# Optimization experiments

Hardware: AMD Instinct MI355X
Metric: run time of the kernel (lower is better)

Reference implementation:

```python
import jax, jax.numpy as jnp
import numpy as np

EPS = 1e-3  # keras LayerNormalization default epsilon

def _layernorm(x, g, b):
    mu = jnp.mean(x, axis=-1, keepdims=True)
    var = jnp.mean(jnp.square(x - mu), axis=-1, keepdims=True)
    return (x - mu) * jax.lax.rsqrt(var + EPS) * g + b

def setup_inputs() -> dict:
    key = jax.random.key(0)
    ks = jax.random.split(key, 12)
    B, T, C = 2, 2048, 768
    s = 0.02
    return {
        "x": jax.random.normal(ks[0], (B, T, C), jnp.float32),
        "ln1_g": jnp.ones((C,), jnp.float32), "ln1_b": jnp.zeros((C,), jnp.float32),
        "Wq": jax.random.normal(ks[1], (C, C), jnp.float32) * s, "bq": jnp.zeros((C,), jnp.float32),
        "Wk": jax.random.normal(ks[2], (C, C), jnp.float32) * s, "bk": jnp.zeros((C,), jnp.float32),
        "Wv": jax.random.normal(ks[3], (C, C), jnp.float32) * s, "bv": jnp.zeros((C,), jnp.float32),
        "ln2_g": jnp.ones((C,), jnp.float32), "ln2_b": jnp.zeros((C,), jnp.float32),
        "W1": jax.random.normal(ks[4], (C, 4 * C), jnp.float32) * s, "b1": jnp.zeros((4 * C,), jnp.float32),
        "W2": jax.random.normal(ks[5], (4 * C, C), jnp.float32) * s, "b2": jnp.zeros((C,), jnp.float32),
    }

def reference(x, ln1_g, ln1_b, Wq, bq, Wk, bk, Wv, bv, ln2_g, ln2_b, W1, b1, W2, b2):
    H = 12
    B, T, C = x.shape
    dh = C // H
    # pre-LN (note: original overwrites x with LN output before residual)
    x = _layernorm(x, ln1_g, ln1_b)
    q = (x @ Wq + bq).reshape(B, T, H, dh).transpose(0, 2, 1, 3)
    k = (x @ Wk + bk).reshape(B, T, H, dh).transpose(0, 2, 1, 3)
    v = (x @ Wv + bv).reshape(B, T, H, dh).transpose(0, 2, 1, 3)
    # original computes K @ Q^T (transpose_b on query)
    scores = jnp.einsum('bhid,bhjd->bhij', k, q) / jnp.sqrt(jnp.float32(dh))
    mask = jnp.tril(jnp.ones((T, T), bool))
    scores = jnp.where(mask, scores, -jnp.inf)
    p = jax.nn.softmax(scores, axis=-1)
    y = jnp.einsum('bhij,bhjd->bhid', p, v)  # [B,H,T,dh]
    y = y.transpose(0, 2, 1, 3).reshape(B, T, C)
    x = x + y
    h = _layernorm(x, ln2_g, ln2_b)
    h = jax.nn.gelu(h @ W1 + b1, approximate=False)
    h = h @ W2 + b2
    return x + h
```

## Files before the change

### kernel.cpp

```cpp
#include <hip/hip_runtime.h>
#include <hip/hip_bf16.h>
#include <cmath>


#define BB 2
#define TT 2048
#define CC 768
#define HH 12
#define DH 64
#define NROWS (BB*TT)
#define NHEADS (BB*HH)

typedef __attribute__((ext_vector_type(8))) short bf16x8;
typedef __attribute__((ext_vector_type(4))) float f32x4;
typedef __attribute__((ext_vector_type(4))) unsigned short u16x4;

__device__ __forceinline__ unsigned short f2bf(float f){
  union { __hip_bfloat16 h; unsigned short u; } c;
  c.h = __float2bfloat16(f);
  return c.u;
}
__device__ __forceinline__ float bf2f(unsigned short u){
  union { unsigned int i; float f; } x; x.i = ((unsigned int)u) << 16; return x.f;
}
template<int BK>
__device__ __forceinline__ int swzk(int r, int c){
  if constexpr (BK == 64) return (r << 6) + (c ^ ((r & 7) << 3));
  else                    return (r << 5) + (c ^ (((r >> 1) & 3) << 3));
}
template<int BK>
__device__ __forceinline__ int swzsrc(int r, int c){
  if constexpr (BK == 64) return c ^ ((r & 7) << 3);
  else                    return c ^ (((r >> 1) & 3) << 3);
}
__device__ __forceinline__ float wred_sum(float v){
  #pragma unroll
  for(int m = 1; m < 64; m <<= 1) v += __shfl_xor(v, m, 64);
  return v;
}
__device__ __forceinline__ float gelu_fast(float x){
  float x2 = x * x;
  float e = x * fmaf(x2, 0.044715f, 1.0f) * 2.30203136f;
  float t = exp2f(e);
  return x - x / (t + 1.0f);
}
__device__ __forceinline__ void gload_lds16(const void* g, void* l){
  __builtin_amdgcn_global_load_lds((const __attribute__((address_space(1))) void*)g,
                                   (__attribute__((address_space(3))) void*)l, 16, 0, 0);
}
template<int N> __device__ __forceinline__ void waitcnt_vm(){
  if constexpr (N == 0)      asm volatile("s_waitcnt vmcnt(0)" ::: "memory");
  else if constexpr (N == 4) asm volatile("s_waitcnt vmcnt(4)" ::: "memory");
  else if constexpr (N == 8) asm volatile("s_waitcnt vmcnt(8)" ::: "memory");
  else static_assert(N == 0 || N == 4 || N == 8, "unsupported vmcnt");
}

#define SCLOG2 (0.125f * 1.44269504f)

__device__ __forceinline__ void tc_body(const float* __restrict__ in,
                                        unsigned short* __restrict__ out,
                                        int K, int N, int bx, int by,
                                        float (*tile)[33]){
  int n0 = bx * 32, k0 = by * 32;
  int t = threadIdx.x; int c = t & 31; int r0 = t >> 5;
  #pragma unroll
  for(int p = 0; p < 4; p++){
    int r = r0 + p * 8;
    tile[r][c] = in[(size_t)(k0 + r) * N + n0 + c];
  }
  __syncthreads();
  #pragma unroll
  for(int p = 0; p < 4; p++){
    int r = r0 + p * 8;
    out[(size_t)(n0 + r) * K + k0 + c] = f2bf(tile[c][r]);
  }
}

__device__ __forceinline__ void ln_body(const float* __restrict__ in,
                                        const float* __restrict__ gm,
                                        const float* __restrict__ bt,
                                        unsigned short* __restrict__ out_b,
                                        int r){
  int t = threadIdx.x;
  const float* row = in + (size_t)r * CC;
  float v0 = row[t], v1 = row[t + 256], v2 = row[t + 512];
  float s = wred_sum(v0 + v1 + v2);
  __shared__ float red[4];
  if((t & 63) == 0) red[t >> 6] = s;
  __syncthreads();
  float mu = (red[0] + red[1] + red[2] + red[3]) * (1.0f / CC);
  float d0 = v0 - mu, d1 = v1 - mu, d2 = v2 - mu;
  float q = wred_sum(d0 * d0 + d1 * d1 + d2 * d2);
  __shared__ float red2[4];
  if((t & 63) == 0) red2[t >> 6] = q;
  __syncthreads();
  float var = (red2[0] + red2[1] + red2[2] + red2[3]) * (1.0f / CC);
  float rinv = rsqrtf(var + 1e-3f);
  float o0 = d0 * rinv * gm[t]       + bt[t];
  float o1 = d1 * rinv * gm[t + 256] + bt[t + 256];
  float o2 = d2 * rinv * gm[t + 512] + bt[t + 512];
  size_t base = (size_t)r * CC;
  out_b[base + t] = f2bf(o0); out_b[base + t + 256] = f2bf(o1); out_b[base + t + 512] = f2bf(o2);
}

__global__ __launch_bounds__(256) void prep_ln_kernel(const float* __restrict__ Wq,
                                                      const float* __restrict__ Wk,
                                                      const float* __restrict__ Wv,
                                                      const float* __restrict__ W1,
                                                      const float* __restrict__ W2,
                                                      const float* __restrict__ bq,
                                                      const float* __restrict__ bk,
                                                      const float* __restrict__ bv,
                                                      const float* __restrict__ x,
                                                      const float* __restrict__ ln1g,
                                                      const float* __restrict__ ln1b,
                                                      unsigned short* __restrict__ wqkv,
                                                      unsigned short* __restrict__ w1t,
                                                      unsigned short* __restrict__ w2t,
                                                      float* __restrict__ bqkv,
                                                      unsigned short* __restrict__ xlnb){
  __shared__ float tile[32][33];
  int o = blockIdx.x;
  if(o < 1728){
    int z = o / 576, r = o % 576;
    const float* in = (z == 0) ? Wq : (z == 1) ? Wk : Wv;
    tc_body(in, wqkv + (size_t)z * CC * CC, CC, CC, r % 24, r / 24, tile);
  } else if(o < 4032){
    int r = o - 1728;
    tc_body(W1, w1t, CC, 4 * CC, r % 96, r / 96, tile);
  } else if(o < 6336){
    int r = o - 4032;
    tc_body(W2, w2t, 4 * CC, CC, r % 24, r / 24, tile);
  } else if(o < 6345){
    int i = (o - 6336) * 256 + threadIdx.x;
    if(i < 3 * CC) bqkv[i] = (i < CC) ? bq[i] : (i < 2 * CC) ? bk[i - CC] : bv[i - 2 * CC];
  } else {
    ln_body(x, ln1g, ln1b, xlnb, o - 6345);
  }
}

template<int MODE, int TILE, int BK>
__global__ __launch_bounds__(256) void gemm_bt(const unsigned short* __restrict__ A,
                                               const unsigned short* __restrict__ Bt,
                                               const float* __restrict__ bias,
                                               const float* __restrict__ resid,
                                               void* __restrict__ outp,
                                               unsigned short* __restrict__ vt,
                                               int M, int N, int K){
  constexpr int F = TILE / 32;
  constexpr int SEGS = TILE * BK / 512;
  constexpr int R = SEGS / 4;
  constexpr int NLD = 2 * R;
  constexpr int LPR = BK / 8;
  constexpr int RPS = 512 / BK;
  __shared__ unsigned short As[3][TILE * BK];
  __shared__ unsigned short Bs[3][TILE * BK];
  int m0 = blockIdx.y * TILE, n0 = blockIdx.x * TILE;
  int t = threadIdx.x; int w = t >> 6; int l = t & 63;
  int g = l >> 4; int lc = l & 15;
  int wm = w >> 1, wn = w & 1;
  f32x4 zero4 = {0.f, 0.f, 0.f, 0.f};
  f32x4 acc[F][F];
  #pragma unroll
  for(int mi = 0; mi < F; mi++)
    #pragma unroll
    for(int ni = 0; ni < F; ni++) acc[mi][ni] = zero4;

  auto stage = [&](int ks, int cb){
    #pragma unroll
    for(int p = 0; p < R; p++){
      int sgi = w * R + p;
      int r = sgi * RPS + l / LPR;
      int c = (l % LPR) * 8;
      int csrc = swzsrc<BK>(r, c);
      gload_lds16(A  + (size_t)(m0 + r) * K + ks + csrc, &As[cb][sgi * 512]);
      gload_lds16(Bt + (size_t)(n0 + r) * K + ks + csrc, &Bs[cb][sgi * 512]);
    }
  };

  int nt = K / BK;
  stage(0, 0);
  if(nt > 1) stage(BK, 1);
  if(nt > 2) stage(2 * BK, 2);
  int cur = 0;
  for(int ti = 0; ti < nt; ti++){
    if(ti + 2 < nt)      waitcnt_vm<2 * NLD>();
    else if(ti + 1 < nt) waitcnt_vm<NLD>();
    else                 waitcnt_vm<0>();
    __builtin_amdgcn_s_barrier();
    #pragma unroll
    for(int kk = 0; kk < BK / 32; kk++){
      bf16x8 af[F], bfv[F];
      #pragma unroll
      for(int mi = 0; mi < F; mi++) af[mi]  = *(const bf16x8*)&As[cur][swzk<BK>(wm * (TILE / 2) + mi * 16 + lc, kk * 32 + g * 8)];
      #pragma unroll
      for(int ni = 0; ni < F; ni++) bfv[ni] = *(const bf16x8*)&Bs[cur][swzk<BK>(wn * (TILE / 2) + ni * 16 + lc, kk * 32 + g * 8)];
      #pragma unroll
      for(int mi = 0; mi < F; mi++)
        #pragma unroll
        for(int ni = 0; ni < F; ni++)
          acc[mi][ni] = __builtin_amdgcn_mfma_f32_16x16x32_bf16(af[mi], bfv[ni], acc[mi][ni], 0, 0, 0);
    }
    __builtin_amdgcn_s_barrier();
    if(ti + 3 < nt) stage((ti + 3) * BK, cur);
    cur = (cur == 2) ? 0 : cur + 1;
  }
  #pragma unroll
  for(int mi = 0; mi < F; mi++)
    #pragma unroll
    for(int ni = 0; ni < F; ni++){
      int col = n0 + wn * (TILE / 2) + ni * 16 + lc;
      float bvv = bias[col];
      if(MODE == 3 && col >= 2 * CC){
        int hh = (col - 2 * CC) >> 6, d = (col - 2 * CC) & 63;
        int rowb = m0 + wm * (TILE / 2) + mi * 16 + g * 4;
        int bb = rowb >> 11, tb = rowb & 2047;
        u16x4 pk;
        #pragma unroll
        for(int rr = 0; rr < 4; rr++) pk[rr] = f2bf(acc[mi][ni][rr] + bvv);
        *(u16x4*)&vt[(((size_t)bb * HH + hh) * DH + d) * TT + tb] = pk;
      } else {
        #pragma unroll
        for(int rr = 0; rr < 4; rr++){
          int row = m0 + wm * (TILE / 2) + mi * 16 + g * 4 + rr;
          float v = acc[mi][ni][rr] + bvv;
          size_t idx = (size_t)row * N + col;
          if(MODE == 2) ((float*)outp)[idx] = v + resid[idx];
          else          ((unsigned short*)outp)[idx] = f2bf(v);
        }
      }
    }
}

__global__ __launch_bounds__(512, 2) void gemm256_gelu(const unsigned short* __restrict__ A,
                                                       const unsigned short* __restrict__ Bt,
                                                       const float* __restrict__ bias,
                                                       unsigned short* __restrict__ outp,
                                                       int M, int N, int K){
  __shared__ unsigned short As[2][256 * 32];
  __shared__ unsigned short Bs[2][256 * 32];
  int m0 = blockIdx.y * 256, n0 = blockIdx.x * 256;
  int t = threadIdx.x; int w = t >> 6; int l = t & 63;
  int g = l >> 4; int lc = l & 15;
  int wm = w >> 2, wn = w & 3;
  f32x4 zero4 = {0.f, 0.f, 0.f, 0.f};
  f32x4 acc[8][4];
  #pragma unroll
  for(int mi = 0; mi < 8; mi++)
    #pragma unroll
    for(int ni = 0; ni < 4; ni++) acc[mi][ni] = zero4;

  auto stage = [&](int ks, int cb){
    #pragma unroll
    for(int p = 0; p < 2; p++){
      int sgi = w * 2 + p;
      int r = sgi * 16 + (l >> 2);
      int c = (l & 3) * 8;
      int csrc = swzsrc<32>(r, c);
      gload_lds16(A  + (size_t)(m0 + r) * K + ks + csrc, &As[cb][sgi * 512]);
      gload_lds16(Bt + (size_t)(n0 + r) * K + ks + csrc, &Bs[cb][sgi * 512]);
    }
  };

  int nt = K >> 5;
  stage(0, 0);
  if(nt > 1) stage(32, 1);
  for(int ti = 0; ti < nt; ti++){
    if(ti + 1 < nt) waitcnt_vm<4>(); else waitcnt_vm<0>();
    __builtin_amdgcn_s_barrier();
    int cur = ti & 1;
    bf16x8 af[8], bfv[4];
    #pragma unroll
    for(int mi = 0; mi < 8; mi++) af[mi]  = *(const bf16x8*)&As[cur][swzk<32>(wm * 128 + mi * 16 + lc, g * 8)];
    #pragma unroll
    for(int ni = 0; ni < 4; ni++) bfv[ni] = *(const bf16x8*)&Bs[cur][swzk<32>(wn * 64 + ni * 16 + lc, g * 8)];
    #pragma unroll
    for(int mi = 0; mi < 8; mi++)
      #pragma unroll
      for(int ni = 0; ni < 4; ni++)
        acc[mi][ni] = __builtin_amdgcn_mfma_f32_16x16x32_bf16(af[mi], bfv[ni], acc[mi][ni], 0, 0, 0);
    __builtin_amdgcn_s_barrier();
    if(ti + 2 < nt) stage((ti + 2) * 32, cur);
  }
  #pragma unroll
  for(int mi = 0; mi < 8; mi++)
    #pragma unroll
    for(int ni = 0; ni < 4; ni++){
      int col = n0 + wn * 64 + ni * 16 + lc;
      float bvv = bias[col];
      #pragma unroll
      for(int rr = 0; rr < 4; rr++){
        int row = m0 + wm * 128 + mi * 16 + g * 4 + rr;
        outp[(size_t)row * N + col] = f2bf(gelu_fast(acc[mi][ni][rr] + bvv));
      }
    }
}

__global__ __launch_bounds__(256) void attn_kernel(const unsigned short* __restrict__ qkv,
                                                   const unsigned short* __restrict__ vt,
                                                   unsigned short* __restrict__ po,
                                                   float* __restrict__ pl,
                                                   float* __restrict__ pm){
  __shared__ unsigned short Aq[2][64 * 64];
  __shared__ unsigned short Vs[2][64 * 64];
  __shared__ unsigned short Ps[4][16 * 64];
  int o = blockIdx.x;
  int xcd = o & 7, qq = o >> 3;
  int head = xcd * 3 + (qq % 3);
  int r_ = qq / 3;
  int bx = 31 - (r_ >> 1);
  int sp = r_ & 1;
  int b = head / HH, h = head % HH;
  int t = threadIdx.x; int w = t >> 6; int l = t & 63;
  int g = l >> 4, lc = l & 15;
  int i0w = bx * 64 + w * 16;
  int irow = i0w + lc;
  unsigned short* pw = &Ps[w][0];

  int hh = (bx + 2) >> 1;
  int js0 = sp ? hh : 0;
  int js1 = sp ? (bx + 1) : hh;

  int rl = l >> 3;
  int csrc = ((l & 7) * 8) ^ (rl * 8);

  bf16x8 bk[2];
  #pragma unroll
  for(int kk = 0; kk < 2; kk++)
    bk[kk] = *(const bf16x8*)(qkv + (size_t)(b * TT + irow) * (3 * CC) + CC + h * DH + kk * 32 + g * 8);

  float m_ = 0.0f, lsum = 0.f;
  f32x4 zero4 = {0.f, 0.f, 0.f, 0.f};
  f32x4 o4[4];
  #pragma unroll
  for(int ds = 0; ds < 4; ds++) o4[ds] = zero4;

  auto stage = [&](int j0, int cb){
    #pragma unroll
    for(int p = 0; p < 2; p++){
      int sgi = w * 2 + p;
      int row = sgi * 8 + rl;
      gload_lds16(qkv + (size_t)(b * TT + j0 + row) * (3 * CC) + h * DH + csrc, &Aq[cb][sgi * 512]);
      gload_lds16(vt  + (size_t)(head * DH + row) * TT + j0 + csrc,             &Vs[cb][sgi * 512]);
    }
  };

  if(js0 < js1){
    stage(js0 * 64, js0 & 1);
    if(js0 + 1 < js1) stage((js0 + 1) * 64, (js0 + 1) & 1);

    for(int jt = js0; jt < js1; jt++){
      int j0 = jt * 64;
      int buf = jt & 1;
      if(jt + 1 < js1) waitcnt_vm<4>(); else waitcnt_vm<0>();
      __builtin_amdgcn_s_barrier();
      f32x4 s[4];
      __builtin_amdgcn_s_setprio(1);
      #pragma unroll
      for(int js = 0; js < 4; js++){
        s[js] = zero4;
        #pragma unroll
        for(int kk = 0; kk < 2; kk++){
          bf16x8 aq = *(const bf16x8*)&Aq[buf][swzk<64>(js * 16 + lc, kk * 32 + g * 8)];
          s[js] = __builtin_amdgcn_mfma_f32_16x16x32_bf16(aq, bk[kk], s[js], 0, 0, 0);
        }
      }
      __builtin_amdgcn_s_setprio(0);
      if(j0 + 63 > i0w){
        #pragma unroll
        for(int js = 0; js < 4; js++)
          #pragma unroll
          for(int rr = 0; rr < 4; rr++){
            int j = j0 + js * 16 + g * 4 + rr;
            if(j > irow) s[js][rr] = -1e30f;
          }
      }
      float nmSC = -m_ * SCLOG2;
      f32x4 p[4];
      float rsum = 0.f;
      #pragma unroll
      for(int js = 0; js < 4; js++)
        #pragma unroll
        for(int rr = 0; rr < 4; rr++){
          float pv = exp2f(fmaf(s[js][rr], SCLOG2, nmSC));
          p[js][rr] = pv;
          rsum += pv;
        }
      rsum += __shfl_xor(rsum, 16, 64);
      rsum += __shfl_xor(rsum, 32, 64);
      if(__builtin_expect(__any(!(rsum < 1e30f)), 0)){
        float mx = -1e30f;
        #pragma unroll
        for(int js = 0; js < 4; js++)
          #pragma unroll
          for(int rr = 0; rr < 4; rr++) mx = fmaxf(mx, s[js][rr]);
        mx = fmaxf(mx, __shfl_xor(mx, 16, 64));
        mx = fmaxf(mx, __shfl_xor(mx, 32, 64));
        float mn = fmaxf(m_, mx);
        float al = exp2f((m_ - mn) * SCLOG2);
        m_ = mn;
        lsum *= al;
        #pragma unroll
        for(int rr = 0; rr < 4; rr++){
          float alb = __shfl(al, g * 4 + rr, 64);
          #pragma unroll
          for(int ds = 0; ds < 4; ds++) o4[ds][rr] *= alb;
        }
        nmSC = -m_ * SCLOG2;
        rsum = 0.f;
        #pragma unroll
        for(int js = 0; js < 4; js++)
          #pragma unroll
          for(int rr = 0; rr < 4; rr++){
            float pv = exp2f(fmaf(s[js][rr], SCLOG2, nmSC));
            p[js][rr] = pv;
            rsum += pv;
          }
        rsum += __shfl_xor(rsum, 16, 64);
        rsum += __shfl_xor(rsum, 32, 64);
      }
      lsum += rsum;
      #pragma unroll
      for(int js = 0; js < 4; js++){
        u16x4 pk;
        #pragma unroll
        for(int rr = 0; rr < 4; rr++) pk[rr] = f2bf(p[js][rr]);
        *(u16x4*)&pw[swzk<64>(lc, js * 16 + g * 4)] = pk;
      }
      bf16x8 pa[2];
      #pragma unroll
      for(int kk = 0; kk < 2; kk++)
        pa[kk] = *(const bf16x8*)&pw[swzk<64>(lc, kk * 32 + g * 8)];
      __builtin_amdgcn_s_setprio(1);
      #pragma unroll
      for(int ds = 0; ds < 4; ds++)
        #pragma unroll
        for(int kk = 0; kk < 2; kk++){
          bf16x8 vb = *(const bf16x8*)&Vs[buf][swzk<64>(ds * 16 + lc, kk * 32 + g * 8)];
          o4[ds] = __builtin_amdgcn_mfma_f32_16x16x32_bf16(pa[kk], vb, o4[ds], 0, 0, 0);
        }
      __builtin_amdgcn_s_setprio(0);
      __builtin_amdgcn_s_barrier();
      if(jt + 2 < js1) stage((jt + 2) * 64, buf);
    }
  }
  size_t pobase = (size_t)sp * (NHEADS * TT * DH) + (size_t)head * TT * DH;
  #pragma unroll
  for(int rr = 0; rr < 4; rr++){
    int ig = i0w + g * 4 + rr;
    #pragma unroll
    for(int ds = 0; ds < 4; ds++)
      po[pobase + (size_t)ig * DH + ds * 16 + lc] = f2bf(o4[ds][rr]);
  }
  if(g == 0){
    size_t pidx = (size_t)sp * (NHEADS * TT) + (size_t)head * TT + i0w + lc;
    pl[pidx] = lsum;
    pm[pidx] = m_;
  }
}

__global__ __launch_bounds__(256) void combine_ln2(const unsigned short* __restrict__ po,
                                                   const float* __restrict__ pl,
                                                   const float* __restrict__ pm,
                                                   const unsigned short* __restrict__ xlnb,
                                                   const float* __restrict__ gm,
                                                   const float* __restrict__ bt,
                                                   float* __restrict__ x1,
                                                   unsigned short* __restrict__ hln2){
  int r = blockIdx.x; int t = threadIdx.x;
  int b = r >> 11, i = r & 2047;
  float v[3];
  #pragma unroll
  for(int p = 0; p < 3; p++){
    int c = t + p * 256;
    int h = c >> 6, d = c & 63;
    size_t pidx = ((size_t)(b * HH + h)) * TT + i;
    float m0v = pm[pidx], m1v = pm[pidx + NHEADS * TT];
    float l0 = pl[pidx],  l1 = pl[pidx + NHEADS * TT];
    float M = fmaxf(m0v, m1v);
    float w0 = exp2f((m0v - M) * SCLOG2), w1 = exp2f((m1v - M) * SCLOG2);
    float p0 = bf2f(po[pidx * DH + d]);
    float p1 = bf2f(po[(size_t)NHEADS * TT * DH + pidx * DH + d]);
    float att = (p0 * w0 + p1 * w1) / (l0 * w0 + l1 * w1);
    v[p] = bf2f(xlnb[(size_t)r * CC + c]) + att;
  }
  float s = wred_sum(v[0] + v[1] + v[2]);
  __shared__ float red[4];
  if((t & 63) == 0) red[t >> 6] = s;
  __syncthreads();
  float mu = (red[0] + red[1] + red[2] + red[3]) * (1.0f / CC);
  float d0 = v[0] - mu, d1 = v[1] - mu, d2 = v[2] - mu;
  float q = wred_sum(d0 * d0 + d1 * d1 + d2 * d2);
  __shared__ float red2[4];
  if((t & 63) == 0) red2[t >> 6] = q;
  __syncthreads();
  float var = (red2[0] + red2[1] + red2[2] + red2[3]) * (1.0f / CC);
  float rinv = rsqrtf(var + 1e-3f);
  size_t base = (size_t)r * CC;
  x1[base + t] = v[0]; x1[base + t + 256] = v[1]; x1[base + t + 512] = v[2];
  hln2[base + t]       = f2bf(d0 * rinv * gm[t]       + bt[t]);
  hln2[base + t + 256] = f2bf(d1 * rinv * gm[t + 256] + bt[t + 256]);
  hln2[base + t + 512] = f2bf(d2 * rinv * gm[t + 512] + bt[t + 512]);
}

extern "C" void kernel_launch(void* const* d_in, const int* in_sizes, int n_in,
                              void* d_out, int out_size, void* d_ws, size_t ws_size,
                              hipStream_t stream){
  const float* x    = (const float*)d_in[0];
  const float* ln1g = (const float*)d_in[1];
  const float* ln1b = (const float*)d_in[2];
  const float* Wq   = (const float*)d_in[3];
  const float* bq   = (const float*)d_in[4];
  const float* Wk   = (const float*)d_in[5];
  const float* bk   = (const float*)d_in[6];
  const float* Wv   = (const float*)d_in[7];
  const float* bv   = (const float*)d_in[8];
  const float* ln2g = (const float*)d_in[9];
  const float* ln2b = (const float*)d_in[10];
  const float* W1   = (const float*)d_in[11];
  const float* b1   = (const float*)d_in[12];
  const float* W2   = (const float*)d_in[13];
  const float* b2   = (const float*)d_in[14];

  char* ws = (char*)d_ws;
  unsigned short* po   = (unsigned short*)(ws + 0);
  unsigned short* xlnb = (unsigned short*)(ws + 12582912);
  float*          x1   = (float*)(ws + 18874368);
  unsigned short* hln2 = (unsigned short*)(ws + 31457280);
  unsigned short* wqkv = (unsigned short*)(ws + 37748736);
  float*          bqkv = (float*)(ws + 41287680);
  unsigned short* w1t  = (unsigned short*)(ws + 41296896);
  unsigned short* w2t  = (unsigned short*)(ws + 46015488);
  unsigned short* qkv  = (unsigned short*)(ws + 50734080);
  unsigned short* vt   = (unsigned short*)(ws + 69608448);
  float*          pl   = (float*)(ws + 75899904);
  float*          pm   = (float*)(ws + 76293120);
  unsigned short* mlp1 = (unsigned short*)(ws + 50734080);

  prep_ln_kernel<<<dim3(6345 + NROWS), 256, 0, stream>>>(Wq, Wk, Wv, W1, W2, bq, bk, bv,
                                                         x, ln1g, ln1b,
                                                         wqkv, w1t, w2t, bqkv, xlnb);

  gemm_bt<3, 128, 32><<<dim3(18, 32), 256, 0, stream>>>(xlnb, wqkv, bqkv, nullptr, qkv, vt, NROWS, 3 * CC, CC);

  attn_kernel<<<dim3(1536), 256, 0, stream>>>(qkv, vt, po, pl, pm);

  combine_ln2<<<dim3(NROWS), 256, 0, stream>>>(po, pl, pm, xlnb, ln2g, ln2b, x1, hln2);

  gemm256_gelu<<<dim3(12, 16), 512, 0, stream>>>(hln2, w1t, b1, mlp1, NROWS, 4 * CC, CC);

  gemm_bt<2, 64, 64><<<dim3(12, 64), 256, 0, stream>>>(mlp1, w2t, b2, x1, d_out, nullptr, NROWS, CC, 4 * CC);

  (void)in_sizes; (void)n_in; (void)out_size; (void)ws_size;
}
```

Measured before the change: 163.2 us.

## Restructure MLP1 GEMM into eight-phase pipelined loop with finer-grained LDS staging

Replaces the two-stage K-loop of the 256x256 GELU GEMM with an 8-phase schedule. Each 64-wide K tile is split into two 32-wide halves, and LDS reads, global-to-LDS loads and MFMA quads are interleaved across phases with barriers and s_setprio around the MFMA blocks. It keeps up to four half-tiles in flight (vmcnt(6)) so global loads, LDS reads and matrix math overlap more tightly. In exchange it adds more barriers per K step and more LDS (2x2x8192 per operand), and it depends on precise waitcnt accounting.

```diff
diff --git a/kernel.cpp b/kernel.cpp
--- a/kernel.cpp
+++ b/kernel.cpp
@@ -51,8 +51,9 @@
 template<int N> __device__ __forceinline__ void waitcnt_vm(){
   if constexpr (N == 0)      asm volatile("s_waitcnt vmcnt(0)" ::: "memory");
   else if constexpr (N == 4) asm volatile("s_waitcnt vmcnt(4)" ::: "memory");
+  else if constexpr (N == 6) asm volatile("s_waitcnt vmcnt(6)" ::: "memory");
   else if constexpr (N == 8) asm volatile("s_waitcnt vmcnt(8)" ::: "memory");
-  else static_assert(N == 0 || N == 4 || N == 8, "unsupported vmcnt");
+  else static_assert(N == 0 || N == 4 || N == 6 || N == 8, "unsupported vmcnt");
 }
 
 #define SCLOG2 (0.125f * 1.44269504f)
@@ -232,13 +233,33 @@
     }
 }
 
-__global__ __launch_bounds__(512, 2) void gemm256_gelu(const unsigned short* __restrict__ A,
-                                                       const unsigned short* __restrict__ Bt,
-                                                       const float* __restrict__ bias,
-                                                       unsigned short* __restrict__ outp,
-                                                       int M, int N, int K){
-  __shared__ unsigned short As[2][256 * 32];
-  __shared__ unsigned short Bs[2][256 * 32];
+#define SWZ32(r, c) (((r) << 5) + ((c) ^ ((((r) >> 1) & 3) << 3)))
+#define MFMA_QUAD(MIB)                                                          \
+  _Pragma("unroll") for(int q = 0; q < 4; q++){                                 \
+    _Pragma("unroll") for(int ni = 0; ni < 4; ni++)                             \
+      acc[(MIB) + q][ni] = __builtin_amdgcn_mfma_f32_16x16x32_bf16(             \
+          af[q], bfv[ni], acc[(MIB) + q][ni], 0, 0, 0); }
+#define LOAD_A(BUF, KH, MIB)                                                    \
+  _Pragma("unroll") for(int q = 0; q < 4; q++)                                  \
+    af[q] = *(const bf16x8*)&As[BUF][KH][SWZ32(wm * 128 + ((MIB) + q) * 16 + lc, g * 8)];
+#define LOAD_B(BUF, KH)                                                         \
+  _Pragma("unroll") for(int q = 0; q < 4; q++)                                  \
+    bfv[q] = *(const bf16x8*)&Bs[BUF][KH][SWZ32(wn * 64 + q * 16 + lc, g * 8)];
+#define PH_TAIL                                                                 \
+  __builtin_amdgcn_s_barrier();                                                 \
+  asm volatile("s_waitcnt lgkmcnt(0)" ::: "memory");                            \
+  __builtin_amdgcn_s_setprio(1);
+#define PH_END                                                                  \
+  __builtin_amdgcn_s_setprio(0);                                                \
+  __builtin_amdgcn_s_barrier();
+
+__global__ __launch_bounds__(512, 2) void gemm256_8ph(const unsigned short* __restrict__ A,
+                                                      const unsigned short* __restrict__ Bt,
+                                                      const float* __restrict__ bias,
+                                                      unsigned short* __restrict__ outp,
+                                                      int M, int N, int K){
+  __shared__ unsigned short As[2][2][8192];
+  __shared__ unsigned short Bs[2][2][8192];
   int m0 = blockIdx.y * 256, n0 = blockIdx.x * 256;
   int t = threadIdx.x; int w = t >> 6; int l = t & 63;
   int g = l >> 4; int lc = l & 15;
@@ -250,37 +271,62 @@
     #pragma unroll
     for(int ni = 0; ni < 4; ni++) acc[mi][ni] = zero4;
 
-  auto stage = [&](int ks, int cb){
+  auto stageH = [&](const unsigned short* __restrict__ X, int rowbase, int kt, int kh,
+                    unsigned short* slot){
     #pragma unroll
     for(int p = 0; p < 2; p++){
-      int sgi = w * 2 + p;
-      int r = sgi * 16 + (l >> 2);
-      int c = (l & 3) * 8;
-      int csrc = swzsrc<32>(r, c);
-      gload_lds16(A  + (size_t)(m0 + r) * K + ks + csrc, &As[cb][sgi * 512]);
-      gload_lds16(Bt + (size_t)(n0 + r) * K + ks + csrc, &Bs[cb][sgi * 512]);
+      int r = p * 128 + (t >> 2);
+      int c = (t & 3) * 8;
+      int csrc = c ^ (((r >> 1) & 3) << 3);
+      gload_lds16(X + (size_t)(rowbase + r) * K + kt * 64 + kh * 32 + csrc,
+                  slot + p * 4096 + w * 512);
     }
   };
 
-  int nt = K >> 5;
-  stage(0, 0);
-  if(nt > 1) stage(32, 1);
-  for(int ti = 0; ti < nt; ti++){
-    if(ti + 1 < nt) waitcnt_vm<4>(); else waitcnt_vm<0>();
-    __builtin_amdgcn_s_barrier();
-    int cur = ti & 1;
-    bf16x8 af[8], bfv[4];
-    #pragma unroll
-    for(int mi = 0; mi < 8; mi++) af[mi]  = *(const bf16x8*)&As[cur][swzk<32>(wm * 128 + mi * 16 + lc, g * 8)];
-    #pragma unroll
-    for(int ni = 0; ni < 4; ni++) bfv[ni] = *(const bf16x8*)&Bs[cur][swzk<32>(wn * 64 + ni * 16 + lc, g * 8)];
-    #pragma unroll
-    for(int mi = 0; mi < 8; mi++)
-      #pragma unroll
-      for(int ni = 0; ni < 4; ni++)
-        acc[mi][ni] = __builtin_amdgcn_mfma_f32_16x16x32_bf16(af[mi], bfv[ni], acc[mi][ni], 0, 0, 0);
-    __builtin_amdgcn_s_barrier();
-    if(ti + 2 < nt) stage((ti + 2) * 32, cur);
+  int nt = K >> 6;
+  int niter = nt >> 1;
+  bf16x8 af[4], bfv[4];
+
+  stageH(A,  m0, 0, 0, &As[0][0][0]);
+  stageH(Bt, n0, 0, 0, &Bs[0][0][0]);
+  stageH(A,  m0, 0, 1, &As[0][1][0]);
+  stageH(Bt, n0, 0, 1, &Bs[0][1][0]);
+  stageH(Bt, n0, 1, 0, &Bs[1][0][0]);
+  stageH(A,  m0, 1, 0, &As[1][0][0]);
+  stageH(Bt, n0, 1, 1, &Bs[1][1][0]);
+  waitcnt_vm<6>();
+  __builtin_amdgcn_s_barrier();
+
+  for(int i = 0; i < niter; i++){
+    int t2 = 2 * i + 2, t3 = 2 * i + 3;
+    bool s2 = t2 < nt, s3 = t3 < nt;
+    bool last = (i == niter - 1);
+    LOAD_A(0, 0, 0) LOAD_B(0, 0)
+    stageH(A, m0, 2 * i + 1, 1, &As[1][1][0]);
+    PH_TAIL MFMA_QUAD(0) PH_END
+    LOAD_A(0, 0, 4)
+    if(s2) stageH(Bt, n0, t2, 0, &Bs[0][0][0]);
+    PH_TAIL MFMA_QUAD(4) PH_END
+    LOAD_A(0, 1, 0) LOAD_B(0, 1)
+    if(s2) stageH(A, m0, t2, 0, &As[0][0][0]);
+    PH_TAIL MFMA_QUAD(0) PH_END
+    LOAD_A(0, 1, 4)
+    if(s2) stageH(Bt, n0, t2, 1, &Bs[0][1][0]);
+    if(last) waitcnt_vm<0>(); else waitcnt_vm<6>();
+    PH_TAIL MFMA_QUAD(4) PH_END
+    LOAD_A(1, 0, 0) LOAD_B(1, 0)
+    if(s2) stageH(A, m0, t2, 1, &As[0][1][0]);
+    PH_TAIL MFMA_QUAD(0) PH_END
+    LOAD_A(1, 0, 4)
+    if(s3) stageH(Bt, n0, t3, 0, &Bs[1][0][0]);
+    PH_TAIL MFMA_QUAD(4) PH_END
+    LOAD_A(1, 1, 0) LOAD_B(1, 1)
+    if(s3) stageH(A, m0, t3, 0, &As[1][0][0]);
+    PH_TAIL MFMA_QUAD(0) PH_END
+    LOAD_A(1, 1, 4)
+    if(s3) stageH(Bt, n0, t3, 1, &Bs[1][1][0]);
+    if(!last) waitcnt_vm<6>();
+    PH_TAIL MFMA_QUAD(4) PH_END
   }
   #pragma unroll
   for(int mi = 0; mi < 8; mi++)
@@ -547,7 +593,7 @@
 
   combine_ln2<<<dim3(NROWS), 256, 0, stream>>>(po, pl, pm, xlnb, ln2g, ln2b, x1, hln2);
 
-  gemm256_gelu<<<dim3(12, 16), 512, 0, stream>>>(hln2, w1t, b1, mlp1, NROWS, 4 * CC, CC);
+  gemm256_8ph<<<dim3(12, 16), 512, 0, stream>>>(hln2, w1t, b1, mlp1, NROWS, 4 * CC, CC);
 
   gemm_bt<2, 64, 64><<<dim3(12, 64), 256, 0, stream>>>(mlp1, w2t, b2, x1, d_out, nullptr, NROWS, CC, 4 * CC);
 
```

Result: faster. 158.7 us (-2.8%).
